# Kernel tuning notes

Measured on AMD Instinct MI355X. Metric: run time of the kernel, lower is better.

The kernel has to match this reference:

```python
import jax, jax.numpy as jnp
import numpy as np

N_EMBD = 1024
N_HEADS = 16
HEAD_DIM = N_EMBD // N_HEADS


def setup_inputs() -> dict:
    key = jax.random.key(0)
    ks = jax.random.split(key, 12)
    B, T, S, C = 2, 2048, 2048, N_EMBD
    std = 1.0 / np.sqrt(C)
    inp = {
        "x": jax.random.normal(ks[0], (B, T, C), dtype=jnp.float32),
        "context": jax.random.normal(ks[1], (B, S, C), dtype=jnp.float32),
        "q_w": jax.random.uniform(ks[2], (C, C), minval=-std, maxval=std, dtype=jnp.float32),
        "q_b": jax.random.uniform(ks[3], (C,), minval=-std, maxval=std, dtype=jnp.float32),
        "k_w": jax.random.uniform(ks[4], (C, C), minval=-std, maxval=std, dtype=jnp.float32),
        "k_b": jax.random.uniform(ks[5], (C,), minval=-std, maxval=std, dtype=jnp.float32),
        "v_w": jax.random.uniform(ks[6], (C, C), minval=-std, maxval=std, dtype=jnp.float32),
        "v_b": jax.random.uniform(ks[7], (C,), minval=-std, maxval=std, dtype=jnp.float32),
        "o_w": jax.random.uniform(ks[8], (C, C), minval=-std, maxval=std, dtype=jnp.float32),
        "o_b": jax.random.uniform(ks[9], (C,), minval=-std, maxval=std, dtype=jnp.float32),
    }
    return inp


def reference(x, context, q_w, q_b, k_w, k_b, v_w, v_b, o_w, o_b):
    B, T, C = x.shape
    S = context.shape[1]
    H, D = N_HEADS, HEAD_DIM
    # projections (torch Linear: y = x @ W^T + b; here weights stored as [in, out])
    q = (x @ q_w + q_b).reshape(B, T, H, D).transpose(0, 2, 1, 3)        # [B,H,T,D]
    k = (context @ k_w + k_b).reshape(B, S, H, D).transpose(0, 2, 1, 3)  # [B,H,S,D]
    v = (context @ v_w + v_b).reshape(B, S, H, D).transpose(0, 2, 1, 3)  # [B,H,S,D]
    att = jnp.einsum("bhtd,bhsd->bhts", q, k) / jnp.sqrt(jnp.float32(D))  # [B,H,T,S]
    causal = jnp.tril(jnp.ones((T, S), dtype=bool))                       # mask from tril buffer
    att = jnp.where(causal[None, None, :, :], att, -jnp.inf)
    att = jax.nn.softmax(att, axis=-1)
    y = jnp.einsum("bhts,bhsd->bhtd", att, v)                             # [B,H,T,D]
    y = y.transpose(0, 2, 1, 3).reshape(B, T, C)
    return y @ o_w + o_b
```

## Files before the change

### kernel.cpp

```cpp
#include <hip/hip_runtime.h>
#include <hip/hip_bf16.h>

using bf16 = __bf16;
using bf16x4 = __attribute__((ext_vector_type(4))) __bf16;
using bf16x8 = __attribute__((ext_vector_type(8))) __bf16;
using f32x4 = __attribute__((ext_vector_type(4))) float;

#define EXP2F(x) __builtin_amdgcn_exp2f(x)

__global__ __launch_bounds__(256) void cvt_kernel(const float4* __restrict__ a,
                                                  const float4* __restrict__ b,
                                                  bf16x4* __restrict__ out) {
  int g = blockIdx.x * blockDim.x + threadIdx.x;
  float4 v = (g < 1048576) ? a[g] : b[g - 1048576];
  bf16x4 o = {(bf16)v.x, (bf16)v.y, (bf16)v.z, (bf16)v.w};
  out[g] = o;
}

__global__ __launch_bounds__(256) void transpose_kernel(const float* __restrict__ w0,
                                                        const float* __restrict__ w1,
                                                        const float* __restrict__ w2,
                                                        const float* __restrict__ w3,
                                                        bf16* __restrict__ wtbase) {
  __shared__ float tile[32][33];
  const int z = blockIdx.z;
  const float* w = (z == 0) ? w0 : (z == 1) ? w1 : (z == 2) ? w2 : w3;
  bf16* wt = wtbase + (size_t)z * 1048576;
  int k0 = blockIdx.y * 32, n0 = blockIdx.x * 32;
  int tx = threadIdx.x, ty = threadIdx.y;
#pragma unroll
  for (int i = 0; i < 4; i++)
    tile[ty + i * 8][tx] = w[(size_t)(k0 + ty + i * 8) * 1024 + n0 + tx];
  __syncthreads();
#pragma unroll
  for (int i = 0; i < 4; i++)
    wt[(size_t)(n0 + ty + i * 8) * 1024 + k0 + tx] = (bf16)tile[tx][ty + i * 8];
}

__device__ __forceinline__ void gemm_body(const bf16* __restrict__ A,
                                          const bf16* __restrict__ Bt,
                                          const float* __restrict__ bias,
                                          void* __restrict__ outp, int mode, int bx, int by) {
  constexpr int K = 1024;
  __shared__ __align__(16) char smem[34816];
  bf16(*As)[40] = (bf16(*)[40])smem;
  bf16(*Bs)[40] = (bf16(*)[40])(smem + 10240);
  bf16(*Cs)[136] = (bf16(*)[136])smem;

  const int tid = threadIdx.x;
  const int lane = tid & 63;
  const int w = tid >> 6;
  const int wr = w >> 1, wc = w & 1;
  const int m0 = by * 128, n0 = bx * 128;
  const int fr = lane & 15, fg = (lane >> 4) * 8;

  f32x4 acc[4][4] = {};

  const int srow = tid >> 2;
  const int kc = (tid & 3) * 8;
  const int arow = m0 + srow, brow = n0 + srow;

  bf16x8 ra0, ra1, rb0, rb1;
  ra0 = *(const bf16x8*)&A[(size_t)arow * K + kc];
  ra1 = *(const bf16x8*)&A[(size_t)(arow + 64) * K + kc];
  rb0 = *(const bf16x8*)&Bt[(size_t)brow * K + kc];
  rb1 = *(const bf16x8*)&Bt[(size_t)(brow + 64) * K + kc];

  for (int k0 = 0; k0 < K; k0 += 32) {
    __syncthreads();
    *(bf16x8*)&As[srow][kc] = ra0;
    *(bf16x8*)&As[srow + 64][kc] = ra1;
    *(bf16x8*)&Bs[srow][kc] = rb0;
    *(bf16x8*)&Bs[srow + 64][kc] = rb1;
    if (k0 + 32 < K) {
      int kn = k0 + 32 + kc;
      ra0 = *(const bf16x8*)&A[(size_t)arow * K + kn];
      ra1 = *(const bf16x8*)&A[(size_t)(arow + 64) * K + kn];
      rb0 = *(const bf16x8*)&Bt[(size_t)brow * K + kn];
      rb1 = *(const bf16x8*)&Bt[(size_t)(brow + 64) * K + kn];
    }
    __syncthreads();
    bf16x8 af[4], bfr[4];
#pragma unroll
    for (int mi = 0; mi < 4; mi++)
      af[mi] = *(const bf16x8*)&As[wr * 64 + mi * 16 + fr][fg];
#pragma unroll
    for (int ni = 0; ni < 4; ni++)
      bfr[ni] = *(const bf16x8*)&Bs[wc * 64 + ni * 16 + fr][fg];
#pragma unroll
    for (int mi = 0; mi < 4; mi++)
#pragma unroll
      for (int ni = 0; ni < 4; ni++)
        acc[mi][ni] =
            __builtin_amdgcn_mfma_f32_16x16x32_bf16(af[mi], bfr[ni], acc[mi][ni], 0, 0, 0);
  }

  float bv[4];
#pragma unroll
  for (int ni = 0; ni < 4; ni++) bv[ni] = bias[n0 + wc * 64 + ni * 16 + fr];
#pragma unroll
  for (int mi = 0; mi < 4; mi++)
#pragma unroll
    for (int ni = 0; ni < 4; ni++)
#pragma unroll
      for (int j = 0; j < 4; j++) acc[mi][ni][j] += bv[ni];

  if (mode == 2) {
    float* O = (float*)outp;
#pragma unroll
    for (int mi = 0; mi < 4; mi++)
#pragma unroll
      for (int ni = 0; ni < 4; ni++)
#pragma unroll
        for (int j = 0; j < 4; j++) {
          int row = m0 + wr * 64 + mi * 16 + (lane >> 4) * 4 + j;
          int col = n0 + wc * 64 + ni * 16 + fr;
          O[(size_t)row * 1024 + col] = acc[mi][ni][j];
        }
    return;
  }

  __syncthreads();
#pragma unroll
  for (int mi = 0; mi < 4; mi++) {
    int r = wr * 64 + mi * 16 + (lane >> 4) * 4;
#pragma unroll
    for (int ni = 0; ni < 4; ni++) {
      int c = wc * 64 + ni * 16 + fr;
#pragma unroll
      for (int j = 0; j < 4; j++) Cs[r + j][c] = (bf16)acc[mi][ni][j];
    }
  }
  __syncthreads();

  bf16* O = (bf16*)outp;
  if (mode == 0) {
    int row = tid >> 1, ch = (tid & 1) * 64;
    int rg = m0 + row;
    int b = rg >> 11, t_ = rg & 2047;
    int c0 = n0 + ch;
    int h = c0 >> 6;
    bf16* dst = O + ((size_t)(b * 16 + h) * 2048 + t_) * 64;
#pragma unroll
    for (int i = 0; i < 8; i++) *(bf16x8*)&dst[i * 8] = *(const bf16x8*)&Cs[row][ch + i * 8];
  } else {
    int colL = tid >> 1, sh = (tid & 1) * 64;
    int cg = n0 + colL;
    int h = cg >> 6, d = cg & 63;
    int rg = m0 + sh;
    int b = rg >> 11, s_ = rg & 2047;
    bf16* dst = O + ((size_t)((b * 16 + h) * 64 + d)) * 2048 + s_;
#pragma unroll
    for (int i = 0; i < 8; i++) {
      bf16x8 v;
#pragma unroll
      for (int jj = 0; jj < 8; jj++) v[jj] = Cs[sh + i * 8 + jj][colL];
      *(bf16x8*)&dst[i * 8] = v;
    }
  }
}

__global__ __launch_bounds__(256) void gemm_qkv_kernel(const bf16* __restrict__ xb,
                                                       const bf16* __restrict__ cb,
                                                       const bf16* __restrict__ wtbase,
                                                       const float* __restrict__ bq,
                                                       const float* __restrict__ bk,
                                                       const float* __restrict__ bv,
                                                       bf16* __restrict__ outbase) {
  const int z = blockIdx.z;
  const bf16* A = (z == 0) ? xb : cb;
  const bf16* Wt = wtbase + (size_t)z * 1048576;
  const float* bias = (z == 0) ? bq : (z == 1) ? bk : bv;
  bf16* out = outbase + (size_t)z * 4194304;
  gemm_body(A, Wt, bias, (void*)out, (z == 2) ? 1 : 0, blockIdx.x, blockIdx.y);
}

__global__ __launch_bounds__(256) void gemm_o_kernel(const bf16* __restrict__ A,
                                                     const bf16* __restrict__ Wt,
                                                     const float* __restrict__ bias,
                                                     float* __restrict__ out) {
  gemm_body(A, Wt, bias, (void*)out, 2, blockIdx.x, blockIdx.y);
}

__global__ __launch_bounds__(256) void attn_kernel(const bf16* __restrict__ Q,
                                                   const bf16* __restrict__ Kc,
                                                   const bf16* __restrict__ Vt,
                                                   bf16* __restrict__ Y) {
  const int bh = blockIdx.x;
  const int qt = 31 - blockIdx.y;
  const int tid = threadIdx.x, lane = tid & 63, w = tid >> 6;
  const int lr = lane & 15, lg = lane >> 4;
  const int q0 = qt * 64 + w * 16;

  __shared__ __align__(16) bf16 Ks[64 * 64];
  __shared__ __align__(16) bf16 Vs[64 * 64];
  __shared__ __align__(16) bf16 Plds[4][16][72];

  const bf16* qb = Q + ((size_t)bh * 2048 + q0 + lr) * 64 + lg * 8;
  const bf16x8 qfB0 = *(const bf16x8*)qb;
  const bf16x8 qfB1 = *(const bf16x8*)(qb + 32);

  const bf16* Kbase = Kc + (size_t)bh * 2048 * 64;
  const bf16* Vbase = Vt + (size_t)bh * 64 * 2048;

  const int srow = tid >> 2;
  const int scol = (tid & 3) * 16;
  const int r7x = (srow & 7) * 8;
  const int d0 = srow * 64 + (scol ^ r7x);
  const int d1 = srow * 64 + ((scol + 8) ^ r7x);

  bf16x8 kr0, kr1, vr0, vr1;
  {
    const bf16* kp = Kbase + (size_t)srow * 64 + scol;
    kr0 = *(const bf16x8*)kp;
    kr1 = *(const bf16x8*)(kp + 8);
    const bf16* vp = Vbase + (size_t)srow * 2048 + scol;
    vr0 = *(const bf16x8*)vp;
    vr1 = *(const bf16x8*)(vp + 8);
  }

  f32x4 yacc[4] = {};
  float mrow = -__builtin_inff(), lrow = 0.0f;
  const float SCL = 0.125f * 1.4426950408889634f;
  const int kxor = (lr & 7) * 8;

  for (int c = 0; c <= qt; ++c) {
    const int sbase = c * 64;
    __syncthreads();
    *(bf16x8*)&Ks[d0] = kr0;
    *(bf16x8*)&Ks[d1] = kr1;
    *(bf16x8*)&Vs[d0] = vr0;
    *(bf16x8*)&Vs[d1] = vr1;
    __syncthreads();

    {
      const int cn = (c < qt) ? c + 1 : c;
      const int sb = cn * 64;
      const bf16* kp = Kbase + (size_t)(sb + srow) * 64 + scol;
      kr0 = *(const bf16x8*)kp;
      kr1 = *(const bf16x8*)(kp + 8);
      const bf16* vp = Vbase + (size_t)srow * 2048 + sb + scol;
      vr0 = *(const bf16x8*)vp;
      vr1 = *(const bf16x8*)(vp + 8);
    }

    f32x4 st[4];
#pragma unroll
    for (int h = 0; h < 4; ++h) {
      const int rb = (16 * h + lr) * 64;
      const bf16x8 kf0 = *(const bf16x8*)&Ks[rb + ((lg * 8) ^ kxor)];
      const bf16x8 kf1 = *(const bf16x8*)&Ks[rb + ((32 + lg * 8) ^ kxor)];
      f32x4 z = {};
      z = __builtin_amdgcn_mfma_f32_16x16x32_bf16(kf0, qfB0, z, 0, 0, 0);
      z = __builtin_amdgcn_mfma_f32_16x16x32_bf16(kf1, qfB1, z, 0, 0, 0);
      st[h] = z;
    }
#pragma unroll
    for (int h = 0; h < 4; ++h)
#pragma unroll
      for (int j = 0; j < 4; ++j) st[h][j] *= SCL;
    if (c == qt) {
      const int qg = q0 + lr;
#pragma unroll
      for (int h = 0; h < 4; ++h)
#pragma unroll
        for (int j = 0; j < 4; ++j) {
          int sg = sbase + 16 * h + lg * 4 + j;
          if (sg > qg) st[h][j] = -__builtin_inff();
        }
    }
    float vmax = fmaxf(fmaxf(st[0][0], st[0][1]), fmaxf(st[0][2], st[0][3]));
#pragma unroll
    for (int h = 1; h < 4; ++h)
      vmax = fmaxf(vmax, fmaxf(fmaxf(st[h][0], st[h][1]), fmaxf(st[h][2], st[h][3])));
    vmax = fmaxf(vmax, __shfl_xor(vmax, 16));
    vmax = fmaxf(vmax, __shfl_xor(vmax, 32));

    if (!__all(vmax <= mrow)) {
      const float mnew = fmaxf(mrow, vmax);
      const float cf = EXP2F(mrow - mnew);
      mrow = mnew;
      lrow *= cf;
      float cfj[4];
#pragma unroll
      for (int j = 0; j < 4; ++j) cfj[j] = __shfl(cf, lg * 4 + j);
#pragma unroll
      for (int nf = 0; nf < 4; ++nf)
#pragma unroll
        for (int j = 0; j < 4; ++j) yacc[nf][j] *= cfj[j];
    }

    float rs = 0.0f;
#pragma unroll
    for (int h = 0; h < 4; ++h) {
      float p0 = EXP2F(st[h][0] - mrow);
      float p1 = EXP2F(st[h][1] - mrow);
      float p2 = EXP2F(st[h][2] - mrow);
      float p3 = EXP2F(st[h][3] - mrow);
      rs += (p0 + p1) + (p2 + p3);
      bf16x4 pk = {(bf16)p0, (bf16)p1, (bf16)p2, (bf16)p3};
      *(bf16x4*)&Plds[w][lr][16 * h + lg * 4] = pk;
    }
    rs += __shfl_xor(rs, 16);
    rs += __shfl_xor(rs, 32);
    lrow += rs;

    const bf16x8 pa0 = *(const bf16x8*)&Plds[w][lr][lg * 8];
    const bf16x8 pa1 = *(const bf16x8*)&Plds[w][lr][32 + lg * 8];
#pragma unroll
    for (int nf = 0; nf < 4; ++nf) {
      const int rb = (nf * 16 + lr) * 64;
      const bf16x8 vf0 = *(const bf16x8*)&Vs[rb + ((lg * 8) ^ kxor)];
      const bf16x8 vf1 = *(const bf16x8*)&Vs[rb + ((32 + lg * 8) ^ kxor)];
      yacc[nf] = __builtin_amdgcn_mfma_f32_16x16x32_bf16(pa0, vf0, yacc[nf], 0, 0, 0);
      yacc[nf] = __builtin_amdgcn_mfma_f32_16x16x32_bf16(pa1, vf1, yacc[nf], 0, 0, 0);
    }
  }

  const float rinv = 1.0f / lrow;
  float linv[4];
#pragma unroll
  for (int j = 0; j < 4; ++j) linv[j] = __shfl(rinv, lg * 4 + j);
  const int b = bh >> 4, h = bh & 15;
#pragma unroll
  for (int nf = 0; nf < 4; ++nf)
#pragma unroll
    for (int j = 0; j < 4; ++j) {
      int qg = q0 + lg * 4 + j;
      Y[((size_t)b * 2048 + qg) * 1024 + h * 64 + nf * 16 + lr] = (bf16)(yacc[nf][j] * linv[j]);
    }
}

extern "C" void kernel_launch(void* const* d_in, const int* in_sizes, int n_in,
                              void* d_out, int out_size, void* d_ws, size_t ws_size,
                              hipStream_t stream) {
  const float* x = (const float*)d_in[0];
  const float* ctx = (const float*)d_in[1];
  const float* q_w = (const float*)d_in[2];
  const float* q_b = (const float*)d_in[3];
  const float* k_w = (const float*)d_in[4];
  const float* k_b = (const float*)d_in[5];
  const float* v_w = (const float*)d_in[6];
  const float* v_b = (const float*)d_in[7];
  const float* o_w = (const float*)d_in[8];
  const float* o_b = (const float*)d_in[9];

  char* ws = (char*)d_ws;
  const size_t MB = 1024 * 1024;
  bf16* xb = (bf16*)(ws + 0);
  bf16* qwt = (bf16*)(ws + 16 * MB);
  bf16* Qws = (bf16*)(ws + 24 * MB);
  bf16* Kws = (bf16*)(ws + 32 * MB);
  bf16* Vt = (bf16*)(ws + 40 * MB);
  bf16* Yws = (bf16*)(ws + 48 * MB);
  bf16* owt = qwt + 3 * 1048576;

  cvt_kernel<<<8192, 256, 0, stream>>>((const float4*)x, (const float4*)ctx, (bf16x4*)xb);

  dim3 tb(32, 8), tg(32, 32, 4);
  transpose_kernel<<<tg, tb, 0, stream>>>(q_w, k_w, v_w, o_w, qwt);

  bf16* cb = xb + (size_t)4096 * 1024 / 2 * 2;
  cb = xb + 4194304;
  gemm_qkv_kernel<<<dim3(8, 32, 3), 256, 0, stream>>>(xb, cb, qwt, q_b, k_b, v_b, Qws);

  attn_kernel<<<dim3(32, 32), 256, 0, stream>>>(Qws, Kws, Vt, Yws);

  gemm_o_kernel<<<dim3(8, 32), 256, 0, stream>>>(Yws, owt, o_b, (float*)d_out);
}
```

Before: 127.1 us.

## Fold softmax scale into Q projection, swizzle GEMM blocks by XCD, raise MFMA priority

The softmax scale (1/sqrt(D)*log2e) moves into the Q projection epilogue, which removes a per-tile multiply in the attention loop. The GEMM launches become 1D grids with an XCD-aware remap, so each XCD works on contiguous tiles and shares L2 better. Templating the GEMM mode removes runtime branches. s_setprio is wrapped around the MFMA sections in attention to favour matrix issue. Q is stored in bf16 after scaling, which may change rounding slightly.

New measurement: 124.1 us. 1.02x faster.

```diff
diff --git a/kernel.cpp b/kernel.cpp
--- a/kernel.cpp
+++ b/kernel.cpp
@@ -37,12 +37,14 @@
     wt[(size_t)(n0 + ty + i * 8) * 1024 + k0 + tx] = (bf16)tile[tx][ty + i * 8];
 }
 
-__device__ __forceinline__ void gemm_body(const bf16* __restrict__ A,
+template <int MODE>
+__device__ __forceinline__ void gemm_body(char* __restrict__ smem,
+                                          const bf16* __restrict__ A,
                                           const bf16* __restrict__ Bt,
                                           const float* __restrict__ bias,
-                                          void* __restrict__ outp, int mode, int bx, int by) {
+                                          void* __restrict__ outp, int bx, int by,
+                                          float oscale) {
   constexpr int K = 1024;
-  __shared__ __align__(16) char smem[34816];
   bf16(*As)[40] = (bf16(*)[40])smem;
   bf16(*Bs)[40] = (bf16(*)[40])(smem + 10240);
   bf16(*Cs)[136] = (bf16(*)[136])smem;
@@ -103,9 +105,9 @@
 #pragma unroll
     for (int ni = 0; ni < 4; ni++)
 #pragma unroll
-      for (int j = 0; j < 4; j++) acc[mi][ni][j] += bv[ni];
-
-  if (mode == 2) {
+      for (int j = 0; j < 4; j++) acc[mi][ni][j] = (acc[mi][ni][j] + bv[ni]) * oscale;
+
+  if (MODE == 2) {
     float* O = (float*)outp;
 #pragma unroll
     for (int mi = 0; mi < 4; mi++)
@@ -134,7 +136,7 @@
   __syncthreads();
 
   bf16* O = (bf16*)outp;
-  if (mode == 0) {
+  if (MODE == 0) {
     int row = tid >> 1, ch = (tid & 1) * 64;
     int rg = m0 + row;
     int b = rg >> 11, t_ = rg & 2047;
@@ -167,19 +169,34 @@
                                                        const float* __restrict__ bk,
                                                        const float* __restrict__ bv,
                                                        bf16* __restrict__ outbase) {
-  const int z = blockIdx.z;
+  __shared__ __align__(16) char smem[34816];
+  const int lin = blockIdx.x;
+  const int xcd = lin & 7, idx = lin >> 3;
+  const int seq = xcd * 96 + idx;
+  const int z = seq >> 8;
+  const int rem = seq & 255;
+  const int by = rem >> 3, bx = rem & 7;
   const bf16* A = (z == 0) ? xb : cb;
   const bf16* Wt = wtbase + (size_t)z * 1048576;
   const float* bias = (z == 0) ? bq : (z == 1) ? bk : bv;
   bf16* out = outbase + (size_t)z * 4194304;
-  gemm_body(A, Wt, bias, (void*)out, (z == 2) ? 1 : 0, blockIdx.x, blockIdx.y);
+  const float oscale = (z == 0) ? 0.125f * 1.4426950408889634f : 1.0f;
+  if (z == 2)
+    gemm_body<1>(smem, A, Wt, bias, (void*)out, bx, by, oscale);
+  else
+    gemm_body<0>(smem, A, Wt, bias, (void*)out, bx, by, oscale);
 }
 
 __global__ __launch_bounds__(256) void gemm_o_kernel(const bf16* __restrict__ A,
                                                      const bf16* __restrict__ Wt,
                                                      const float* __restrict__ bias,
                                                      float* __restrict__ out) {
-  gemm_body(A, Wt, bias, (void*)out, 2, blockIdx.x, blockIdx.y);
+  __shared__ __align__(16) char smem[34816];
+  const int lin = blockIdx.x;
+  const int xcd = lin & 7, idx = lin >> 3;
+  const int seq = xcd * 32 + idx;
+  const int by = seq >> 3, bx = seq & 7;
+  gemm_body<2>(smem, A, Wt, bias, (void*)out, bx, by, 1.0f);
 }
 
 __global__ __launch_bounds__(256) void attn_kernel(const bf16* __restrict__ Q,
@@ -221,7 +238,6 @@
 
   f32x4 yacc[4] = {};
   float mrow = -__builtin_inff(), lrow = 0.0f;
-  const float SCL = 0.125f * 1.4426950408889634f;
   const int kxor = (lr & 7) * 8;
 
   for (int c = 0; c <= qt; ++c) {
@@ -245,6 +261,7 @@
     }
 
     f32x4 st[4];
+    __builtin_amdgcn_s_setprio(1);
 #pragma unroll
     for (int h = 0; h < 4; ++h) {
       const int rb = (16 * h + lr) * 64;
@@ -255,10 +272,7 @@
       z = __builtin_amdgcn_mfma_f32_16x16x32_bf16(kf1, qfB1, z, 0, 0, 0);
       st[h] = z;
     }
-#pragma unroll
-    for (int h = 0; h < 4; ++h)
-#pragma unroll
-      for (int j = 0; j < 4; ++j) st[h][j] *= SCL;
+    __builtin_amdgcn_s_setprio(0);
     if (c == qt) {
       const int qg = q0 + lr;
 #pragma unroll
@@ -307,6 +321,7 @@
 
     const bf16x8 pa0 = *(const bf16x8*)&Plds[w][lr][lg * 8];
     const bf16x8 pa1 = *(const bf16x8*)&Plds[w][lr][32 + lg * 8];
+    __builtin_amdgcn_s_setprio(1);
 #pragma unroll
     for (int nf = 0; nf < 4; ++nf) {
       const int rb = (nf * 16 + lr) * 64;
@@ -315,6 +330,7 @@
       yacc[nf] = __builtin_amdgcn_mfma_f32_16x16x32_bf16(pa0, vf0, yacc[nf], 0, 0, 0);
       yacc[nf] = __builtin_amdgcn_mfma_f32_16x16x32_bf16(pa1, vf1, yacc[nf], 0, 0, 0);
     }
+    __builtin_amdgcn_s_setprio(0);
   }
 
   const float rinv = 1.0f / lrow;
@@ -354,17 +370,16 @@
   bf16* Vt = (bf16*)(ws + 40 * MB);
   bf16* Yws = (bf16*)(ws + 48 * MB);
   bf16* owt = qwt + 3 * 1048576;
+  bf16* cb = xb + 4194304;
 
   cvt_kernel<<<8192, 256, 0, stream>>>((const float4*)x, (const float4*)ctx, (bf16x4*)xb);
 
   dim3 tb(32, 8), tg(32, 32, 4);
   transpose_kernel<<<tg, tb, 0, stream>>>(q_w, k_w, v_w, o_w, qwt);
 
-  bf16* cb = xb + (size_t)4096 * 1024 / 2 * 2;
-  cb = xb + 4194304;
-  gemm_qkv_kernel<<<dim3(8, 32, 3), 256, 0, stream>>>(xb, cb, qwt, q_b, k_b, v_b, Qws);
+  gemm_qkv_kernel<<<768, 256, 0, stream>>>(xb, cb, qwt, q_b, k_b, v_b, Qws);
 
   attn_kernel<<<dim3(32, 32), 256, 0, stream>>>(Qws, Kws, Vt, Yws);
 
-  gemm_o_kernel<<<dim3(8, 32), 256, 0, stream>>>(Yws, owt, o_b, (float*)d_out);
-}
+  gemm_o_kernel<<<256, 256, 0, stream>>>(Yws, owt, o_b, (float*)d_out);
+}
```
